# Performance work log

Hardware: AMD Instinct MI355X
Metric: run time of the kernel (lower is better)

## Reference

```python
import jax, jax.numpy as jnp
import numpy as np

N, H, E = 16384, 256, 4096  # nodes, hubs, embedding_size


def setup_inputs() -> dict:
    key = jax.random.key(0)
    ks = jax.random.split(key, 6)
    node_embeddings = jax.random.normal(ks[0], (N, E), dtype=jnp.float32)
    hub_indices = jnp.sort(jax.random.randint(ks[1], (H,), 0, N, dtype=jnp.int64))
    Wq = jax.random.normal(ks[2], (E, E), dtype=jnp.float32) * 0.02
    bq = jnp.zeros((E,), dtype=jnp.float32)
    Wk = jax.random.normal(ks[3], (E, E), dtype=jnp.float32) * 0.02
    bk = jnp.zeros((E,), dtype=jnp.float32)
    return {"node_embeddings": node_embeddings, "hub_indices": hub_indices,
            "Wq": Wq, "bq": bq, "Wk": Wk, "bk": bk}


def reference(node_embeddings, hub_indices, Wq, bq, Wk, bk):
    # Batched version of the original per-node Python loop.
    hub_emb = node_embeddings[hub_indices]                      # [H, E]
    Q = node_embeddings @ Wq.T + bq                             # [N, E]
    K = hub_emb @ Wk.T + bk                                     # [H, E]
    scale = 1.0 / np.sqrt(E).astype(np.float32)
    scores = (Q @ K.T) * scale                                  # [N, H]
    # softmax is monotonic, so argmax(softmax(scores)) == argmax(scores);
    # the original's value/context computation is dead code w.r.t. the output.
    best_hub = hub_indices[jnp.argmax(scores, axis=-1)]         # [N]
    node_ids = jnp.arange(N, dtype=hub_indices.dtype)
    is_hub = jnp.isin(node_ids, hub_indices)                    # [N] bool
    assignments = jnp.where(is_hub, node_ids, best_hub)
    return assignments
```

## Files before the change

kernel.cpp:

```cpp
#include <hip/hip_runtime.h>

#define E  4096
#define NN 16384
#define HH 256
#define WL_CAP 2048
#define REF_SLOTS 256
#define QT 16
#define MARGIN 0.0625f

typedef __attribute__((ext_vector_type(4))) float f32x4;
typedef __attribute__((ext_vector_type(8))) short bf16x8;

static __device__ __forceinline__ unsigned short f2bf(float f) {
    unsigned int u = __float_as_uint(f);
    u += 0x7fffu + ((u >> 16) & 1u);
    return (unsigned short)(u >> 16);
}
static __device__ __forceinline__ float bf2f(unsigned short h) {
    return __uint_as_float((unsigned int)h << 16);
}

__global__ void init_kernel(int* cnt) { if (threadIdx.x == 0) *cnt = 0; }

__global__ __launch_bounds__(256) void k_proj64_kernel(
    const float* __restrict__ X, const int* __restrict__ hub,
    const float* __restrict__ Wk, const float* __restrict__ bk,
    double* __restrict__ K64, double* __restrict__ K64T)
{
    __shared__ double As[16][68];
    __shared__ double Bs[16][68];
    __shared__ int rows[64];

    const int t  = threadIdx.x;
    const int m0 = blockIdx.y * 64;
    const int n0 = blockIdx.x * 64;

    if (t < 64) rows[t] = hub[m0 + t];
    __syncthreads();

    const int tx = t & 15, ty = t >> 4;
    const int kI = (t & 3) * 4, rr = t >> 2;

    double acc[4][4] = {};

    for (int k0 = 0; k0 < E; k0 += 16) {
        const float4 a4 = *(const float4*)&X[(size_t)rows[rr] * E + k0 + kI];
        As[kI + 0][rr] = (double)a4.x; As[kI + 1][rr] = (double)a4.y;
        As[kI + 2][rr] = (double)a4.z; As[kI + 3][rr] = (double)a4.w;
        const float4 b4 = *(const float4*)&Wk[(size_t)(n0 + rr) * E + k0 + kI];
        Bs[kI + 0][rr] = (double)b4.x; Bs[kI + 1][rr] = (double)b4.y;
        Bs[kI + 2][rr] = (double)b4.z; Bs[kI + 3][rr] = (double)b4.w;
        __syncthreads();
#pragma unroll
        for (int k = 0; k < 16; ++k) {
            double av[4], bv[4];
#pragma unroll
            for (int i = 0; i < 4; ++i) av[i] = As[k][ty * 4 + i];
#pragma unroll
            for (int j = 0; j < 4; ++j) bv[j] = Bs[k][tx * 4 + j];
#pragma unroll
            for (int i = 0; i < 4; ++i)
#pragma unroll
                for (int j = 0; j < 4; ++j)
                    acc[i][j] = fma(av[i], bv[j], acc[i][j]);
        }
        __syncthreads();
    }

#pragma unroll
    for (int i = 0; i < 4; ++i)
#pragma unroll
        for (int j = 0; j < 4; ++j) {
            const double v = acc[i][j] + (double)bk[n0 + tx * 4 + j];
            K64 [(size_t)(m0 + ty * 4 + i) * E  + n0 + tx * 4 + j] = v;
            K64T[(size_t)(n0 + tx * 4 + j) * HH + m0 + ty * 4 + i] = v;
        }
}

__global__ __launch_bounds__(256) void s_proj32_kernel(
    const double* __restrict__ K64, const float* __restrict__ Wq,
    unsigned short* __restrict__ Sh, unsigned short* __restrict__ Sl)
{
    __shared__ float As[32][68];
    __shared__ float Bs[32][68];

    const int t  = threadIdx.x;
    const int m0 = blockIdx.y * 64;
    const int n0 = blockIdx.x * 64;
    const int tx = t & 15, ty = t >> 4;

    const int ar  = t >> 2, aq = (t & 3) * 8;
    const int bkk = t >> 3, bn = (t & 7) * 8;

    float acc[4][4] = {};

    for (int k0 = 0; k0 < E; k0 += 32) {
        {
            const double* ap = &K64[(size_t)(m0 + ar) * E + k0 + aq];
#pragma unroll
            for (int i = 0; i < 4; ++i) {
                const double2 d2 = *(const double2*)(ap + 2 * i);
                As[aq + 2 * i + 0][ar] = (float)d2.x;
                As[aq + 2 * i + 1][ar] = (float)d2.y;
            }
        }
        {
            const float4 b0 = *(const float4*)&Wq[(size_t)(k0 + bkk) * E + n0 + bn];
            const float4 b1 = *(const float4*)&Wq[(size_t)(k0 + bkk) * E + n0 + bn + 4];
            Bs[bkk][bn + 0] = b0.x; Bs[bkk][bn + 1] = b0.y;
            Bs[bkk][bn + 2] = b0.z; Bs[bkk][bn + 3] = b0.w;
            Bs[bkk][bn + 4] = b1.x; Bs[bkk][bn + 5] = b1.y;
            Bs[bkk][bn + 6] = b1.z; Bs[bkk][bn + 7] = b1.w;
        }
        __syncthreads();
#pragma unroll
        for (int k = 0; k < 32; ++k) {
            float av[4], bv[4];
#pragma unroll
            for (int i = 0; i < 4; ++i) av[i] = As[k][ty * 4 + i];
#pragma unroll
            for (int j = 0; j < 4; ++j) bv[j] = Bs[k][tx * 4 + j];
#pragma unroll
            for (int i = 0; i < 4; ++i)
#pragma unroll
                for (int j = 0; j < 4; ++j)
                    acc[i][j] = fmaf(av[i], bv[j], acc[i][j]);
        }
        __syncthreads();
    }

#pragma unroll
    for (int i = 0; i < 4; ++i) {
        const int h = m0 + ty * 4 + i;
        ushort4 h4, l4;
        float s;
        s = acc[i][0]; h4.x = f2bf(s); l4.x = f2bf(s - bf2f(h4.x));
        s = acc[i][1]; h4.y = f2bf(s); l4.y = f2bf(s - bf2f(h4.y));
        s = acc[i][2]; h4.z = f2bf(s); l4.z = f2bf(s - bf2f(h4.z));
        s = acc[i][3]; h4.w = f2bf(s); l4.w = f2bf(s - bf2f(h4.w));
        *(ushort4*)&Sh[(size_t)h * E + n0 + tx * 4] = h4;
        *(ushort4*)&Sl[(size_t)h * E + n0 + tx * 4] = l4;
    }
}

__global__ __launch_bounds__(256) void cvec32_kernel(
    const float* __restrict__ bq, const double* __restrict__ K64,
    float* __restrict__ c32)
{
    const int h = blockIdx.x;
    const int t = threadIdx.x;
    double s = 0.0;
    for (int e = t; e < E; e += 256)
        s = fma((double)bq[e], K64[(size_t)h * E + e], s);
#pragma unroll
    for (int m = 32; m; m >>= 1) s += __shfl_down(s, m, 64);
    __shared__ double red[4];
    if ((t & 63) == 0) red[t >> 6] = s;
    __syncthreads();
    if (t == 0) c32[h] = (float)(red[0] + red[1] + red[2] + red[3]);
}

__global__ __launch_bounds__(512) void scores_mfma_kernel(
    const float* __restrict__ X,
    const unsigned short* __restrict__ Sh, const unsigned short* __restrict__ Sl,
    const float* __restrict__ c32, const int* __restrict__ hub,
    int* __restrict__ out, int* __restrict__ cnt, int* __restrict__ wl)
{
    __shared__ __align__(16) unsigned short Ah[64][40];
    __shared__ __align__(16) unsigned short Al[64][40];
    __shared__ __align__(16) unsigned short Bh[256][40];
    __shared__ __align__(16) unsigned short Bl[256][40];
    __shared__ float bias[256];
    __shared__ float mv1[4][64];
    __shared__ float mv2[4][64];
    __shared__ int   mi1[4][64];

    const int t    = threadIdx.x;
    const int m0   = blockIdx.x * 64;
    const int lane = t & 63;
    const int w    = t >> 6;
    const int wm   = w >> 2;
    const int wn   = w & 3;
    const int lr   = lane & 15;
    const int lg   = lane >> 4;

    const int arow = t >> 3;
    const int akc  = (t & 7) * 4;

    if (t < 256) {
        const bool dup = (t > 0) && (hub[t - 1] == hub[t]);
        bias[t] = dup ? -3.4e38f : c32[t];
    }

    f32x4 acc[2][4] = {};

    for (int k0 = 0; k0 < E; k0 += 32) {
        {
            const float4 a4 = *(const float4*)&X[(size_t)(m0 + arow) * E + k0 + akc];
            ushort4 h4, l4;
            h4.x = f2bf(a4.x); l4.x = f2bf(a4.x - bf2f(h4.x));
            h4.y = f2bf(a4.y); l4.y = f2bf(a4.y - bf2f(h4.y));
            h4.z = f2bf(a4.z); l4.z = f2bf(a4.z - bf2f(h4.z));
            h4.w = f2bf(a4.w); l4.w = f2bf(a4.w - bf2f(h4.w));
            *(ushort4*)&Ah[arow][akc] = h4;
            *(ushort4*)&Al[arow][akc] = l4;
        }
#pragma unroll
        for (int rep = 0; rep < 2; ++rep) {
            const int c   = t + rep * 512;
            const int row = c >> 2;
            const int kq  = (c & 3) * 8;
            *(uint4*)&Bh[row][kq] = *(const uint4*)&Sh[(size_t)row * E + k0 + kq];
            *(uint4*)&Bl[row][kq] = *(const uint4*)&Sl[(size_t)row * E + k0 + kq];
        }
        __syncthreads();

        bf16x8 a_h[2], a_l[2], b_h[4], b_l[4];
#pragma unroll
        for (int im = 0; im < 2; ++im) {
            const int row = wm * 32 + im * 16 + lr;
            a_h[im] = *(const bf16x8*)&Ah[row][lg * 8];
            a_l[im] = *(const bf16x8*)&Al[row][lg * 8];
        }
#pragma unroll
        for (int in = 0; in < 4; ++in) {
            const int row = wn * 64 + in * 16 + lr;
            b_h[in] = *(const bf16x8*)&Bh[row][lg * 8];
            b_l[in] = *(const bf16x8*)&Bl[row][lg * 8];
        }
#pragma unroll
        for (int im = 0; im < 2; ++im)
#pragma unroll
            for (int in = 0; in < 4; ++in)
                acc[im][in] = __builtin_amdgcn_mfma_f32_16x16x32_bf16(
                    a_h[im], b_h[in], acc[im][in], 0, 0, 0);
#pragma unroll
        for (int im = 0; im < 2; ++im)
#pragma unroll
            for (int in = 0; in < 4; ++in)
                acc[im][in] = __builtin_amdgcn_mfma_f32_16x16x32_bf16(
                    a_h[im], b_l[in], acc[im][in], 0, 0, 0);
#pragma unroll
        for (int im = 0; im < 2; ++im)
#pragma unroll
            for (int in = 0; in < 4; ++in)
                acc[im][in] = __builtin_amdgcn_mfma_f32_16x16x32_bf16(
                    a_l[im], b_h[in], acc[im][in], 0, 0, 0);
        __syncthreads();
    }

    float cr[4];
#pragma unroll
    for (int in = 0; in < 4; ++in) cr[in] = bias[wn * 64 + in * 16 + lr];

#pragma unroll
    for (int im = 0; im < 2; ++im) {
#pragma unroll
        for (int r = 0; r < 4; ++r) {
            float v1 = -3.4e38f, v2 = -3.4e38f;
            int   i1 = 0;
#pragma unroll
            for (int in = 0; in < 4; ++in) {
                const float v = acc[im][in][r] + cr[in];
                if (v > v1)      { v2 = v1; v1 = v; i1 = wn * 64 + in * 16 + lr; }
                else if (v > v2) { v2 = v; }
            }
#pragma unroll
            for (int m = 8; m; m >>= 1) {
                const float ov1 = __shfl_xor(v1, m, 64);
                const int   oi1 = __shfl_xor(i1, m, 64);
                const float ov2 = __shfl_xor(v2, m, 64);
                if (ov1 > v1 || (ov1 == v1 && oi1 < i1)) {
                    v2 = fmaxf(v1, ov2); v1 = ov1; i1 = oi1;
                } else {
                    v2 = fmaxf(v2, ov1);
                }
            }
            if (lr == 0) {
                const int nl = wm * 32 + im * 16 + lg * 4 + r;
                mv1[wn][nl] = v1; mi1[wn][nl] = i1; mv2[wn][nl] = v2;
            }
        }
    }
    __syncthreads();

    if (t < 64) {
        float v1 = -3.4e38f, v2 = -3.4e38f;
        int   i1 = 0x7fffffff;
#pragma unroll
        for (int wq = 0; wq < 4; ++wq) {
            const float a1 = mv1[wq][t];
            const int   ai = mi1[wq][t];
            const float a2 = mv2[wq][t];
            if (a1 > v1 || (a1 == v1 && ai < i1)) {
                v2 = fmaxf(v2, v1); v1 = a1; i1 = ai; v2 = fmaxf(v2, a2);
            } else {
                v2 = fmaxf(v2, a1);
            }
        }
        const int node = m0 + t;
        out[node] = hub[i1];
        if (v1 - v2 < MARGIN) {
            const int idx = atomicAdd(cnt, 1);
            if (idx < WL_CAP) wl[idx] = node;
        }
    }
}

__global__ __launch_bounds__(256) void refine_q_kernel(
    const float* __restrict__ X, const float* __restrict__ Wq,
    const float* __restrict__ bq, const int* __restrict__ cnt,
    const int* __restrict__ wl, double* __restrict__ Q64)
{
    const int n = min(min(*cnt, WL_CAP), REF_SLOTS);
    const int slot0 = blockIdx.y * QT;
    if (slot0 >= n) return;
    const int ep0 = blockIdx.x * 64;
    const int t = threadIdx.x;

    __shared__ int rows[QT];
    __shared__ float As[32][QT + 4];
    __shared__ float Bs[32][68];
    if (t < QT) rows[t] = wl[min(slot0 + t, n - 1)];
    __syncthreads();

    const int r  = t >> 4;
    const int cg = (t & 15) * 4;

    double acc[4] = {0.0, 0.0, 0.0, 0.0};

    for (int k0 = 0; k0 < E; k0 += 32) {
        if (t < 128) {
            const int ar = t >> 3, kc = (t & 7) * 4;
            const float4 a4 = *(const float4*)&X[(size_t)rows[ar] * E + k0 + kc];
            As[kc + 0][ar] = a4.x; As[kc + 1][ar] = a4.y;
            As[kc + 2][ar] = a4.z; As[kc + 3][ar] = a4.w;
        }
        {
            const int br = t >> 2, kc = (t & 3) * 8;
            const float4 b0 = *(const float4*)&Wq[(size_t)(ep0 + br) * E + k0 + kc];
            const float4 b1 = *(const float4*)&Wq[(size_t)(ep0 + br) * E + k0 + kc + 4];
            Bs[kc + 0][br] = b0.x; Bs[kc + 1][br] = b0.y;
            Bs[kc + 2][br] = b0.z; Bs[kc + 3][br] = b0.w;
            Bs[kc + 4][br] = b1.x; Bs[kc + 5][br] = b1.y;
            Bs[kc + 6][br] = b1.z; Bs[kc + 7][br] = b1.w;
        }
        __syncthreads();
#pragma unroll
        for (int k = 0; k < 32; ++k) {
            const double a = (double)As[k][r];
#pragma unroll
            for (int j = 0; j < 4; ++j)
                acc[j] = fma(a, (double)Bs[k][cg + j], acc[j]);
        }
        __syncthreads();
    }
#pragma unroll
    for (int j = 0; j < 4; ++j)
        Q64[(size_t)(slot0 + r) * E + ep0 + cg + j] = acc[j] + (double)bq[ep0 + cg + j];
}

__global__ __launch_bounds__(256) void refine_partial_kernel(
    const double* __restrict__ Q64, const double* __restrict__ K64T,
    const int* __restrict__ cnt, const int* __restrict__ wl,
    double* __restrict__ partials)
{
    const int slot = blockIdx.y;
    const int n = min(min(*cnt, WL_CAP), REF_SLOTS);
    if (slot >= n) return;

    const int t  = threadIdx.x;
    const int c  = blockIdx.x;
    const int e0 = c * 512;

    __shared__ __align__(16) double Qs[512];
    if (t < 128) {
        const double2 q0 = *(const double2*)&Q64[(size_t)slot * E + e0 + t * 4];
        const double2 q1 = *(const double2*)&Q64[(size_t)slot * E + e0 + t * 4 + 2];
        Qs[t * 4 + 0] = q0.x; Qs[t * 4 + 1] = q0.y;
        Qs[t * 4 + 2] = q1.x; Qs[t * 4 + 3] = q1.y;
    }
    __syncthreads();

    double a0 = 0, a1 = 0, a2 = 0, a3 = 0;
    for (int e = 0; e < 512; e += 4) {
        const size_t base = (size_t)(e0 + e) * HH + t;
        a0 = fma(Qs[e + 0], K64T[base + 0 * HH], a0);
        a1 = fma(Qs[e + 1], K64T[base + 1 * HH], a1);
        a2 = fma(Qs[e + 2], K64T[base + 2 * HH], a2);
        a3 = fma(Qs[e + 3], K64T[base + 3 * HH], a3);
    }
    partials[((size_t)slot * 8 + c) * HH + t] = (a0 + a1) + (a2 + a3);
}

__global__ __launch_bounds__(256) void refine_reduce_kernel(
    const double* __restrict__ partials, const int* __restrict__ hub,
    const int* __restrict__ cnt, const int* __restrict__ wl,
    int* __restrict__ out)
{
    const int slot = blockIdx.x;
    const int n = min(min(*cnt, WL_CAP), REF_SLOTS);
    if (slot >= n) return;

    const int t = threadIdx.x;
    double v = 0.0;
#pragma unroll
    for (int c = 0; c < 8; ++c)
        v += partials[((size_t)slot * 8 + c) * HH + t];

    __shared__ double rv[256];
    __shared__ int    ri[256];
    rv[t] = v; ri[t] = t;
    __syncthreads();
    for (int s = 128; s; s >>= 1) {
        if (t < s) {
            const bool better = rv[t + s] > rv[t] ||
                                (rv[t + s] == rv[t] && ri[t + s] < ri[t]);
            if (better) { rv[t] = rv[t + s]; ri[t] = ri[t + s]; }
        }
        __syncthreads();
    }
    if (t == 0) out[wl[slot]] = hub[ri[0]];
}

__global__ void hub_override_kernel(const int* __restrict__ hub,
                                    int* __restrict__ out)
{
    const int t = threadIdx.x;
    if (t < HH) { const int h = hub[t]; out[h] = h; }
}

extern "C" void kernel_launch(void* const* d_in, const int* in_sizes, int n_in,
                              void* d_out, int out_size, void* d_ws, size_t ws_size,
                              hipStream_t stream) {
    const float* X   = (const float*)d_in[0];
    const int*   hub = (const int*)  d_in[1];
    const float* Wq  = (const float*)d_in[2];
    const float* bq  = (const float*)d_in[3];
    const float* Wk  = (const float*)d_in[4];
    const float* bk  = (const float*)d_in[5];
    int* out = (int*)d_out;

    double*         K64  = (double*)d_ws;
    double*         K64T = K64 + (size_t)HH * E;
    unsigned short* Sh   = (unsigned short*)(K64T + (size_t)HH * E);
    unsigned short* Sl   = Sh + (size_t)HH * E;
    float*          c32  = (float*)(Sl + (size_t)HH * E);
    int*            cnt  = (int*)(c32 + HH);
    int*            wl   = cnt + 1;
    double*         Q64  = K64;
    double*         partials = (double*)Sh;

    init_kernel<<<dim3(1), 64, 0, stream>>>(cnt);
    k_proj64_kernel<<<dim3(E / 64, HH / 64), 256, 0, stream>>>(X, hub, Wk, bk, K64, K64T);
    s_proj32_kernel<<<dim3(E / 64, HH / 64), 256, 0, stream>>>(K64, Wq, Sh, Sl);
    cvec32_kernel<<<dim3(HH), 256, 0, stream>>>(bq, K64, c32);
    scores_mfma_kernel<<<dim3(NN / 64), 512, 0, stream>>>(X, Sh, Sl, c32, hub, out, cnt, wl);
    refine_q_kernel<<<dim3(E / 64, REF_SLOTS / QT), 256, 0, stream>>>(X, Wq, bq, cnt, wl, Q64);
    refine_partial_kernel<<<dim3(8, REF_SLOTS), 256, 0, stream>>>(Q64, K64T, cnt, wl, partials);
    refine_reduce_kernel<<<dim3(REF_SLOTS), 256, 0, stream>>>(partials, hub, cnt, wl, out);
    hub_override_kernel<<<dim3(1), 256, 0, stream>>>(hub, out);
}
```

Baseline: 1.538 ms.

## Split-K the hub key projection and move S projection onto bf16 MFMA

The fp64 key projection for the hubs, which only launches 256 blocks, is split along K into up to 8 slabs when the workspace is large enough. A separate reduce kernel sums the slabs, adds the bias, and writes both K64 and its transpose. The S = K·Wq projection replaces scalar fp32 FMAs with split-bf16 (hi/lo, three-term) MFMA instructions. This trades extra workspace traffic and a reduction pass, plus slightly different S precision, for more parallelism and matrix-core throughput.

```diff
diff --git a/kernel.cpp b/kernel.cpp
--- a/kernel.cpp
+++ b/kernel.cpp
@@ -8,8 +8,8 @@
 #define QT 16
 #define MARGIN 0.0625f
 
-typedef __attribute__((ext_vector_type(4))) float f32x4;
-typedef __attribute__((ext_vector_type(8))) short bf16x8;
+typedef __attribute__((ext_vector_type(4))) float  f32x4;
+typedef __attribute__((ext_vector_type(8))) short  bf16x8;
 
 static __device__ __forceinline__ unsigned short f2bf(float f) {
     unsigned int u = __float_as_uint(f);
@@ -77,70 +77,191 @@
         }
 }
 
-__global__ __launch_bounds__(256) void s_proj32_kernel(
-    const double* __restrict__ K64, const float* __restrict__ Wq,
-    unsigned short* __restrict__ Sh, unsigned short* __restrict__ Sl)
-{
-    __shared__ float As[32][68];
-    __shared__ float Bs[32][68];
+__global__ __launch_bounds__(256) void k_proj_part_kernel(
+    const float* __restrict__ X, const int* __restrict__ hub,
+    const float* __restrict__ Wk, int kspan, double* __restrict__ part)
+{
+    __shared__ double As[16][68];
+    __shared__ double Bs[16][68];
+    __shared__ int rows[64];
 
     const int t  = threadIdx.x;
     const int m0 = blockIdx.y * 64;
     const int n0 = blockIdx.x * 64;
+    const int kbeg = blockIdx.z * kspan;
+
+    if (t < 64) rows[t] = hub[m0 + t];
+    __syncthreads();
+
     const int tx = t & 15, ty = t >> 4;
-
-    const int ar  = t >> 2, aq = (t & 3) * 8;
-    const int bkk = t >> 3, bn = (t & 7) * 8;
-
-    float acc[4][4] = {};
+    const int kI = (t & 3) * 4, rr = t >> 2;
+
+    double acc[4][4] = {};
+
+    for (int k0 = kbeg; k0 < kbeg + kspan; k0 += 16) {
+        const float4 a4 = *(const float4*)&X[(size_t)rows[rr] * E + k0 + kI];
+        As[kI + 0][rr] = (double)a4.x; As[kI + 1][rr] = (double)a4.y;
+        As[kI + 2][rr] = (double)a4.z; As[kI + 3][rr] = (double)a4.w;
+        const float4 b4 = *(const float4*)&Wk[(size_t)(n0 + rr) * E + k0 + kI];
+        Bs[kI + 0][rr] = (double)b4.x; Bs[kI + 1][rr] = (double)b4.y;
+        Bs[kI + 2][rr] = (double)b4.z; Bs[kI + 3][rr] = (double)b4.w;
+        __syncthreads();
+#pragma unroll
+        for (int k = 0; k < 16; ++k) {
+            double av[4], bv[4];
+#pragma unroll
+            for (int i = 0; i < 4; ++i) av[i] = As[k][ty * 4 + i];
+#pragma unroll
+            for (int j = 0; j < 4; ++j) bv[j] = Bs[k][tx * 4 + j];
+#pragma unroll
+            for (int i = 0; i < 4; ++i)
+#pragma unroll
+                for (int j = 0; j < 4; ++j)
+                    acc[i][j] = fma(av[i], bv[j], acc[i][j]);
+        }
+        __syncthreads();
+    }
+
+#pragma unroll
+    for (int i = 0; i < 4; ++i)
+#pragma unroll
+        for (int j = 0; j < 4; ++j)
+            part[(size_t)blockIdx.z * HH * E +
+                 (size_t)(m0 + ty * 4 + i) * E + n0 + tx * 4 + j] = acc[i][j];
+}
+
+__global__ __launch_bounds__(256) void k_reduce_kernel(
+    const double* __restrict__ part, const float* __restrict__ bk,
+    int ks, double* __restrict__ K64, double* __restrict__ K64T)
+{
+    __shared__ double tile[64][65];
+    const int t  = threadIdx.x;
+    const int e0 = blockIdx.x * 64, h0 = blockIdx.y * 64;
+
+#pragma unroll
+    for (int rep = 0; rep < 16; ++rep) {
+        const int idx = rep * 256 + t;
+        const int lh = idx >> 6, le = idx & 63;
+        const size_t off = (size_t)(h0 + lh) * E + e0 + le;
+        double s = part[off];
+        for (int z = 1; z < ks; ++z) s += part[(size_t)z * HH * E + off];
+        const double v = s + (double)bk[e0 + le];
+        K64[off] = v;
+        tile[lh][le] = v;
+    }
+    __syncthreads();
+#pragma unroll
+    for (int rep = 0; rep < 16; ++rep) {
+        const int idx = rep * 256 + t;
+        const int le = idx >> 6, lh = idx & 63;
+        K64T[(size_t)(e0 + le) * HH + h0 + lh] = tile[lh][le];
+    }
+}
+
+__global__ __launch_bounds__(256) void s_proj_mfma_kernel(
+    const double* __restrict__ K64, const float* __restrict__ Wq,
+    unsigned short* __restrict__ Sh, unsigned short* __restrict__ Sl)
+{
+    __shared__ __align__(16) unsigned short Ah[64][40];
+    __shared__ __align__(16) unsigned short Al[64][40];
+    __shared__ __align__(16) float Bf[32][72];
+
+    const int t  = threadIdx.x;
+    const int m0 = blockIdx.y * 64;
+    const int n0 = blockIdx.x * 64;
+
+    const int lane = t & 63;
+    const int w    = t >> 6;
+    const int wr   = w >> 1;
+    const int wc   = w & 1;
+    const int lr   = lane & 15;
+    const int lg   = lane >> 4;
+
+    const int arow = t >> 2;
+    const int akc  = (t & 3) * 8;
+    const int bkr  = t >> 3;
+    const int bnc  = (t & 7) * 8;
+
+    f32x4 acc[2][2] = {};
 
     for (int k0 = 0; k0 < E; k0 += 32) {
         {
-            const double* ap = &K64[(size_t)(m0 + ar) * E + k0 + aq];
-#pragma unroll
-            for (int i = 0; i < 4; ++i) {
-                const double2 d2 = *(const double2*)(ap + 2 * i);
-                As[aq + 2 * i + 0][ar] = (float)d2.x;
-                As[aq + 2 * i + 1][ar] = (float)d2.y;
+            const double* ap = &K64[(size_t)(m0 + arow) * E + k0 + akc];
+#pragma unroll
+            for (int q = 0; q < 2; ++q) {
+                const double2 d0 = *(const double2*)(ap + 4 * q);
+                const double2 d1 = *(const double2*)(ap + 4 * q + 2);
+                const float f0 = (float)d0.x, f1 = (float)d0.y;
+                const float f2 = (float)d1.x, f3 = (float)d1.y;
+                ushort4 hh, ll;
+                hh.x = f2bf(f0); ll.x = f2bf(f0 - bf2f(hh.x));
+                hh.y = f2bf(f1); ll.y = f2bf(f1 - bf2f(hh.y));
+                hh.z = f2bf(f2); ll.z = f2bf(f2 - bf2f(hh.z));
+                hh.w = f2bf(f3); ll.w = f2bf(f3 - bf2f(hh.w));
+                *(ushort4*)&Ah[arow][akc + 4 * q] = hh;
+                *(ushort4*)&Al[arow][akc + 4 * q] = ll;
             }
         }
         {
-            const float4 b0 = *(const float4*)&Wq[(size_t)(k0 + bkk) * E + n0 + bn];
-            const float4 b1 = *(const float4*)&Wq[(size_t)(k0 + bkk) * E + n0 + bn + 4];
-            Bs[bkk][bn + 0] = b0.x; Bs[bkk][bn + 1] = b0.y;
-            Bs[bkk][bn + 2] = b0.z; Bs[bkk][bn + 3] = b0.w;
-            Bs[bkk][bn + 4] = b1.x; Bs[bkk][bn + 5] = b1.y;
-            Bs[bkk][bn + 6] = b1.z; Bs[bkk][bn + 7] = b1.w;
-        }
-        __syncthreads();
-#pragma unroll
-        for (int k = 0; k < 32; ++k) {
-            float av[4], bv[4];
-#pragma unroll
-            for (int i = 0; i < 4; ++i) av[i] = As[k][ty * 4 + i];
-#pragma unroll
-            for (int j = 0; j < 4; ++j) bv[j] = Bs[k][tx * 4 + j];
-#pragma unroll
-            for (int i = 0; i < 4; ++i)
-#pragma unroll
-                for (int j = 0; j < 4; ++j)
-                    acc[i][j] = fmaf(av[i], bv[j], acc[i][j]);
-        }
-        __syncthreads();
-    }
-
-#pragma unroll
-    for (int i = 0; i < 4; ++i) {
-        const int h = m0 + ty * 4 + i;
-        ushort4 h4, l4;
-        float s;
-        s = acc[i][0]; h4.x = f2bf(s); l4.x = f2bf(s - bf2f(h4.x));
-        s = acc[i][1]; h4.y = f2bf(s); l4.y = f2bf(s - bf2f(h4.y));
-        s = acc[i][2]; h4.z = f2bf(s); l4.z = f2bf(s - bf2f(h4.z));
-        s = acc[i][3]; h4.w = f2bf(s); l4.w = f2bf(s - bf2f(h4.w));
-        *(ushort4*)&Sh[(size_t)h * E + n0 + tx * 4] = h4;
-        *(ushort4*)&Sl[(size_t)h * E + n0 + tx * 4] = l4;
-    }
+            const float* wp = &Wq[(size_t)(k0 + bkr) * E + n0 + bnc];
+            *(float4*)&Bf[bkr][bnc]     = *(const float4*)wp;
+            *(float4*)&Bf[bkr][bnc + 4] = *(const float4*)(wp + 4);
+        }
+        __syncthreads();
+
+        bf16x8 a_h[2], a_l[2], b_h[2], b_l[2];
+#pragma unroll
+        for (int im = 0; im < 2; ++im) {
+            const int row = wr * 32 + im * 16 + lr;
+            a_h[im] = *(const bf16x8*)&Ah[row][lg * 8];
+            a_l[im] = *(const bf16x8*)&Al[row][lg * 8];
+        }
+#pragma unroll
+        for (int in = 0; in < 2; ++in) {
+            const int col = wc * 32 + in * 16 + lr;
+#pragma unroll
+            for (int j = 0; j < 8; ++j) {
+                const float f = Bf[lg * 8 + j][col];
+                const unsigned short bh = f2bf(f);
+                b_h[in][j] = (short)bh;
+                b_l[in][j] = (short)f2bf(f - bf2f(bh));
+            }
+        }
+#pragma unroll
+        for (int im = 0; im < 2; ++im)
+#pragma unroll
+            for (int in = 0; in < 2; ++in)
+                acc[im][in] = __builtin_amdgcn_mfma_f32_16x16x32_bf16(
+                    a_h[im], b_h[in], acc[im][in], 0, 0, 0);
+#pragma unroll
+        for (int im = 0; im < 2; ++im)
+#pragma unroll
+            for (int in = 0; in < 2; ++in)
+                acc[im][in] = __builtin_amdgcn_mfma_f32_16x16x32_bf16(
+                    a_h[im], b_l[in], acc[im][in], 0, 0, 0);
+#pragma unroll
+        for (int im = 0; im < 2; ++im)
+#pragma unroll
+            for (int in = 0; in < 2; ++in)
+                acc[im][in] = __builtin_amdgcn_mfma_f32_16x16x32_bf16(
+                    a_l[im], b_h[in], acc[im][in], 0, 0, 0);
+        __syncthreads();
+    }
+
+#pragma unroll
+    for (int im = 0; im < 2; ++im)
+#pragma unroll
+        for (int in = 0; in < 2; ++in) {
+            const int kc = n0 + wc * 32 + in * 16 + lr;
+#pragma unroll
+            for (int r = 0; r < 4; ++r) {
+                const int h = m0 + wr * 32 + im * 16 + 4 * lg + r;
+                const float s = acc[im][in][r];
+                const unsigned short sh = f2bf(s);
+                Sh[(size_t)h * E + kc] = sh;
+                Sl[(size_t)h * E + kc] = f2bf(s - bf2f(sh));
+            }
+        }
 }
 
 __global__ __launch_bounds__(256) void cvec32_kernel(
@@ -449,15 +570,31 @@
     int*            cnt  = (int*)(c32 + HH);
     int*            wl   = cnt + 1;
     double*         Q64  = K64;
-    double*         partials = (double*)Sh;
+    double*         rpart = (double*)Sh;
+
+    const size_t BASE = 21000192;
+    const size_t slab = (size_t)HH * E * sizeof(double);
+    int ks = 1;
+    if      (ws_size >= BASE + 8 * slab) ks = 8;
+    else if (ws_size >= BASE + 4 * slab) ks = 4;
+    else if (ws_size >= BASE + 2 * slab) ks = 2;
+    double* kpart = (double*)((char*)d_ws + BASE);
 
     init_kernel<<<dim3(1), 64, 0, stream>>>(cnt);
-    k_proj64_kernel<<<dim3(E / 64, HH / 64), 256, 0, stream>>>(X, hub, Wk, bk, K64, K64T);
-    s_proj32_kernel<<<dim3(E / 64, HH / 64), 256, 0, stream>>>(K64, Wq, Sh, Sl);
+    if (ks > 1) {
+        k_proj_part_kernel<<<dim3(E / 64, HH / 64, ks), 256, 0, stream>>>(
+            X, hub, Wk, E / ks, kpart);
+        k_reduce_kernel<<<dim3(E / 64, HH / 64), 256, 0, stream>>>(
+            kpart, bk, ks, K64, K64T);
+    } else {
+        k_proj64_kernel<<<dim3(E / 64, HH / 64), 256, 0, stream>>>(
+            X, hub, Wk, bk, K64, K64T);
+    }
+    s_proj_mfma_kernel<<<dim3(E / 64, HH / 64), 256, 0, stream>>>(K64, Wq, Sh, Sl);
     cvec32_kernel<<<dim3(HH), 256, 0, stream>>>(bq, K64, c32);
     scores_mfma_kernel<<<dim3(NN / 64), 512, 0, stream>>>(X, Sh, Sl, c32, hub, out, cnt, wl);
     refine_q_kernel<<<dim3(E / 64, REF_SLOTS / QT), 256, 0, stream>>>(X, Wq, bq, cnt, wl, Q64);
-    refine_partial_kernel<<<dim3(8, REF_SLOTS), 256, 0, stream>>>(Q64, K64T, cnt, wl, partials);
-    refine_reduce_kernel<<<dim3(REF_SLOTS), 256, 0, stream>>>(partials, hub, cnt, wl, out);
+    refine_partial_kernel<<<dim3(8, REF_SLOTS), 256, 0, stream>>>(Q64, K64T, cnt, wl, rpart);
+    refine_reduce_kernel<<<dim3(REF_SLOTS), 256, 0, stream>>>(rpart, hub, cnt, wl, out);
     hub_override_kernel<<<dim3(1), 256, 0, stream>>>(hub, out);
 }
```

New measurement: 1.336 ms. -13.1%, faster.
